# Optimization experiments

Hardware: AMD Instinct MI355X
Metric: run time of the kernel (lower is better)

Reference implementation:

```python
import jax, jax.numpy as jnp
import numpy as np

B, F, Q, CHUNK = 2, 8192, 4096, 512
NUM_VERTS = 6000


def _safe_div(n, d):
    return n / jnp.where(d == 0, 1.0, d)


def _bary(a, b, c, p):
    """Barycentric coords of the closest point on triangle (a,b,c) to p.
    All args broadcastable [..., 3]; returns [..., 3] (u, v, w) with
    closest = u*a + v*b + w*c. Ericson, Real-Time Collision Detection."""
    ab = b - a; ac = c - a; ap = p - a
    d1 = jnp.sum(ab * ap, -1); d2 = jnp.sum(ac * ap, -1)
    bp = p - b
    d3 = jnp.sum(ab * bp, -1); d4 = jnp.sum(ac * bp, -1)
    cp_ = p - c
    d5 = jnp.sum(ab * cp_, -1); d6 = jnp.sum(ac * cp_, -1)
    vc = d1 * d4 - d3 * d2
    vb = d5 * d2 - d1 * d6
    va = d3 * d6 - d5 * d4
    v_ab = _safe_div(d1, d1 - d3)
    w_ac = _safe_div(d2, d2 - d6)
    w_bc = _safe_div(d4 - d3, (d4 - d3) + (d5 - d6))
    inv = _safe_div(1.0, va + vb + vc)
    v_in = vb * inv; w_in = vc * inv
    zero = jnp.zeros_like(d1); one = jnp.ones_like(d1)
    conds = [(d1 <= 0) & (d2 <= 0),
             (d3 >= 0) & (d4 <= d3),
             (vc <= 0) & (d1 >= 0) & (d3 <= 0),
             (d6 >= 0) & (d5 <= d6),
             (vb <= 0) & (d2 >= 0) & (d6 <= 0),
             (va <= 0) & (d4 >= d3) & (d5 >= d6)]
    u = jnp.select(conds, [one, zero, 1 - v_ab, zero, 1 - w_ac, zero], 1 - v_in - w_in)
    v = jnp.select(conds, [zero, one, v_ab, zero, zero, 1 - w_bc], v_in)
    w = jnp.select(conds, [zero, zero, zero, one, w_ac, w_bc], w_in)
    return jnp.stack([u, v, w], -1)


def _closest_faces(triangles, points, chunk=CHUNK):
    """Exact closest-triangle index per query point (replaces BVH search).
    triangles [B,F,3,3], points [B,Q,3] -> int32 [B,Q]."""
    tri = jax.lax.stop_gradient(triangles)
    pts = jax.lax.stop_gradient(points)
    bsz, nq = pts.shape[0], pts.shape[1]
    a = tri[:, :, 0]; b = tri[:, :, 1]; c = tri[:, :, 2]  # [B,F,3]

    def one_chunk(p_chunk):  # [B,CH,3]
        pa = p_chunk[:, :, None, :]                       # [B,CH,1,3]
        bc = _bary(a[:, None], b[:, None], c[:, None], pa)  # [B,CH,F,3]
        cp = (bc[..., 0:1] * a[:, None] + bc[..., 1:2] * b[:, None]
              + bc[..., 2:3] * c[:, None])                # [B,CH,F,3]
        d2 = jnp.sum((cp - pa) ** 2, -1)                  # [B,CH,F]
        return jnp.argmin(d2, axis=-1)                    # [B,CH]

    chunks = jnp.moveaxis(pts.reshape(bsz, nq // chunk, chunk, 3), 1, 0)
    idx = jax.lax.map(one_chunk, chunks)                  # [NC,B,CH]
    return jnp.moveaxis(idx, 0, 1).reshape(bsz, nq)


def setup_inputs() -> dict:
    key = jax.random.key(0)
    k1, k2, k3, k4, k5 = jax.random.split(key, 5)
    return {
        'triangles': jax.random.normal(k1, (B, F, 3, 3), dtype=jnp.float32),
        'points': jax.random.normal(k2, (B, Q, 3), dtype=jnp.float32),
        'normals': jax.random.normal(k3, (B, F, 3, 3), dtype=jnp.float32),
        'cmaps': jax.random.normal(k4, (B, F, 3, 3), dtype=jnp.float32),
        'faces': jax.random.randint(k5, (B, F, 3), 0, NUM_VERTS, dtype=jnp.int32),
    }


def reference(triangles, points, normals, cmaps, faces):
    closest_faces = _closest_faces(triangles, points)     # [B,Q]
    idx = closest_faces[:, :, None, None]
    tri_g = jnp.take_along_axis(triangles, idx, axis=1)   # [B,Q,3,3]
    nrm_g = jnp.take_along_axis(normals, idx, axis=1)
    cmp_g = jnp.take_along_axis(cmaps, idx, axis=1)
    bcs = _bary(tri_g[:, :, 0], tri_g[:, :, 1], tri_g[:, :, 2], points)  # [B,Q,3]
    bcs = jnp.clip(bcs, 0.0, 1.0)
    closest_points = jnp.einsum('bqk,bqkd->bqd', bcs, tri_g)
    closest_normals = jnp.einsum('bqk,bqkd->bqd', bcs, nrm_g)
    closest_cmaps = jnp.einsum('bqk,bqkd->bqd', bcs, cmp_g)
    residual = closest_points - points
    closest_fids = jnp.take_along_axis(faces, closest_faces[:, :, None], axis=1)  # [B,Q,3]
    closest_idx = jnp.take_along_axis(
        closest_fids, jnp.argmax(bcs, -1)[:, :, None], axis=2)[..., 0]            # [B,Q]
    return residual, closest_normals, closest_cmaps, closest_idx
```

## Files before the change

kernel.cpp:

```cpp
#include <hip/hip_runtime.h>
#include <float.h>

#define B_   2
#define F_   8192
#define Q_   4096
#define NC   128
#define FC   (F_/NC)
#define PTS  256
#define PPT  2

typedef float f2 __attribute__((ext_vector_type(2)));
typedef unsigned int uint;

__device__ __forceinline__ f2 clamp01(f2 x) {
    f2 z = {0.f, 0.f}, o = {1.f, 1.f};
    return __builtin_elementwise_min(__builtin_elementwise_max(x, z), o);
}

__device__ __forceinline__ void bary_uvw(
    float ax, float ay, float az,
    float bx, float by, float bz,
    float cx, float cy, float cz,
    float px, float py, float pz,
    float& u, float& v, float& w)
{
#pragma clang fp contract(off)
    float abx = bx - ax, aby = by - ay, abz = bz - az;
    float acx = cx - ax, acy = cy - ay, acz = cz - az;
    float apx = px - ax, apy = py - ay, apz = pz - az;
    float d1 = abx*apx + aby*apy + abz*apz;
    float d2 = acx*apx + acy*apy + acz*apz;
    float bpx = px - bx, bpy = py - by, bpz = pz - bz;
    float d3 = abx*bpx + aby*bpy + abz*bpz;
    float d4 = acx*bpx + acy*bpy + acz*bpz;
    float qx = px - cx, qy = py - cy, qz = pz - cz;
    float d5 = abx*qx + aby*qy + abz*qz;
    float d6 = acx*qx + acy*qy + acz*qz;
    float vc = d1*d4 - d3*d2;
    float vb = d5*d2 - d1*d6;
    float va = d3*d6 - d5*d4;

    bool c1 = (d1 <= 0.f) && (d2 <= 0.f);
    bool c2 = (d3 >= 0.f) && (d4 <= d3);
    bool c3 = (vc <= 0.f) && (d1 >= 0.f) && (d3 <= 0.f);
    bool c4 = (d6 >= 0.f) && (d5 <= d6);
    bool c5 = (vb <= 0.f) && (d2 >= 0.f) && (d6 <= 0.f);
    bool c6 = (va <= 0.f) && (d4 >= d3) && (d5 >= d6);

    bool e1 = c1;
    bool p1 = !c1;
    bool e2 = p1 && c2;
    bool p2 = p1 && !c2;
    bool e3 = p2 && c3;
    bool p3 = p2 && !c3;
    bool e4 = p3 && c4;
    bool p4 = p3 && !c4;
    bool e5 = p4 && c5;
    bool p5 = p4 && !c5;
    bool e6 = p5 && c6;

    float d43 = d4 - d3;
    float d56 = d5 - d6;
    float n  = e3 ? d1        : (e5 ? d2        : (e6 ? d43         : 1.f));
    float dd = e3 ? (d1 - d3) : (e5 ? (d2 - d6) : (e6 ? (d43 + d56) : (va + vb + vc)));
    dd = (dd == 0.f) ? 1.f : dd;
    float t = n / dd;

    float vi = vb * t;
    float wi = vc * t;
    u = e1 ? 1.f : (e2 ? 0.f : (e3 ? 1.f - t : (e4 ? 0.f : (e5 ? 1.f - t : (e6 ? 0.f     : 1.f - vi - wi)))));
    v = e1 ? 0.f : (e2 ? 1.f : (e3 ? t       : (e4 ? 0.f : (e5 ? 0.f     : (e6 ? 1.f - t : vi)))));
    w = e1 ? 0.f : (e2 ? 0.f : (e3 ? 0.f     : (e4 ? 1.f : (e5 ? t       : (e6 ? t       : wi)))));
}

__global__ __launch_bounds__(PTS, 8) void scan_kernel(
    const float* __restrict__ tri, const float* __restrict__ pts,
    uint2* __restrict__ keys)
{
    __shared__ float4 S[FC * 4];
    const int tid = threadIdx.x;
    const int pb = blockIdx.x, cb = blockIdx.y, bb = blockIdx.z;

    {
        const int tr = tid & (FC - 1);
        const int qt = tid >> 6;
        const float* g = tri + ((size_t)bb * F_ + (size_t)cb * FC + tr) * 9;
        float ax = g[0], ay = g[1], az = g[2];
        float bx = g[3], by = g[4], bz = g[5];
        float cx = g[6], cy = g[7], cz = g[8];
        float abx = bx - ax, aby = by - ay, abz = bz - az;
        float acx = cx - ax, acy = cy - ay, acz = cz - az;
        float daa = abx*abx + aby*aby + abz*abz;
        float dcc = acx*acx + acy*acy + acz*acz;
        float dac = abx*acx + aby*acy + abz*acz;
        float4 v;
        if (qt == 0)      v = make_float4(ax, ay, az, daa);
        else if (qt == 1) v = make_float4(abx, aby, abz, dcc);
        else if (qt == 2) v = make_float4(acx, acy, acz, dac);
        else {
            float dbc = daa + dcc - 2.f*dac;
            float nn  = daa*dcc - dac*dac;
            v = make_float4(1.f/daa, 1.f/dcc, 1.f/dbc, 1.f/nn);
        }
        S[tr*4 + qt] = v;
    }
    __syncthreads();

    const int q0 = pb * (PTS * PPT) + tid * PPT;
    const float* p0 = pts + ((size_t)bb * Q_ + q0) * 3;
    f2 px = {p0[0], p0[3]};
    f2 py = {p0[1], p0[4]};
    f2 pz = {p0[2], p0[5]};

    uint a0 = 0xFFFFFFFFu, a1 = 0xFFFFFFFFu;
    uint b0 = 0xFFFFFFFFu, b1 = 0xFFFFFFFFu;
    #pragma unroll 2
    for (int fl = 0; fl < FC; ++fl) {
        float4 c0 = S[fl*4 + 0];
        float4 c1 = S[fl*4 + 1];
        float4 c2 = S[fl*4 + 2];
        float4 c3 = S[fl*4 + 3];
        float daa = c0.w, dcc = c1.w, dac = c2.w;
        float dbc = daa + dcc - 2.f*dac;
        float nn  = daa*dcc - dac*dac;
        float kk  = daa - dac;

        f2 apx = px - c0.x, apy = py - c0.y, apz = pz - c0.z;
        f2 d1  = c1.x*apx + c1.y*apy + c1.z*apz;
        f2 d2  = c2.x*apx + c2.y*apy + c2.z*apz;
        f2 app = apx*apx + apy*apy + apz*apz;
        f2 t1  = d1*dcc - d2*dac;
        f2 t2  = d2*daa - d1*dac;
        f2 t12 = t1 + t2;
        f2 sg  = d1*t1 + d2*t2;
        f2 dint = app - sg*c3.w;

        f2 d43 = (d2 - d1) + kk;
        f2 td1 = d1 + d1;
        f2 tab = clamp01(d1 * c3.x);
        f2 eab = app - tab*(td1 - tab*daa);
        f2 tac = clamp01(d2 * c3.y);
        f2 eac = app - tac*((d2 + d2) - tac*dcc);
        f2 bpp = (app - td1) + daa;
        f2 sbc = clamp01(d43 * c3.z);
        f2 ebc = bpp - sbc*((d43 + d43) - sbc*dbc);
        f2 emin = __builtin_elementwise_min(__builtin_elementwise_min(eab, eac), ebc);

        bool inA = (t1.x >= 0.f) & (t2.x >= 0.f) & (t12.x <= nn);
        bool inB = (t1.y >= 0.f) & (t2.y >= 0.f) & (t12.y <= nn);
        float dA = fmaxf(inA ? dint.x : emin.x, 0.f);
        float dB = fmaxf(inB ? dint.y : emin.y, 0.f);

        uint kA = (__float_as_uint(dA) & 0xFFFFFFC0u) | (uint)fl;
        uint kB = (__float_as_uint(dB) & 0xFFFFFFC0u) | (uint)fl;
        uint lo = min(a0, kA), hi = max(a0, kA);
        a0 = lo; a1 = min(a1, hi);
        lo = min(b0, kB); hi = max(b0, kB);
        b0 = lo; b1 = min(b1, hi);
    }

    size_t o = ((size_t)bb * Q_ + q0) * NC + cb;
    keys[o]      = make_uint2(a0, a1);
    keys[o + NC] = make_uint2(b0, b1);
}

__global__ __launch_bounds__(256) void finalize_kernel(
    const float* __restrict__ tri, const float* __restrict__ pts,
    const float* __restrict__ nrm, const float* __restrict__ cmp,
    const int* __restrict__ faces,
    const uint* __restrict__ keys,
    float* __restrict__ out)
{
#pragma clang fp contract(off)
    const int lane = threadIdx.x & 63;
    const int t = blockIdx.x * 4 + (threadIdx.x >> 6);
    const int bb = t / Q_;

    const float* pp = pts + (size_t)t * 3;
    float px = pp[0], py = pp[1], pz = pp[2];

    const uint4* kp = (const uint4*)keys;
    uint4 K = kp[(size_t)t * (NC/2) + lane];

    float dbest = FLT_MAX; int fbest = 0x7FFFFFFF;
    uint kj[4] = {K.x, K.y, K.z, K.w};
    #pragma unroll
    for (int j = 0; j < 4; ++j) {
        int face = (2*lane + (j >> 1)) * FC + (int)(kj[j] & 63u);
        const float* tg = tri + ((size_t)bb * F_ + face) * 9;
        float ax = tg[0], ay = tg[1], az = tg[2];
        float bx = tg[3], by = tg[4], bz = tg[5];
        float cx = tg[6], cy = tg[7], cz = tg[8];
        float u, v, w;
        bary_uvw(ax, ay, az, bx, by, bz, cx, cy, cz, px, py, pz, u, v, w);
        float cpx = u*ax + v*bx + w*cx;
        float cpy = u*ay + v*by + w*cy;
        float cpz = u*az + v*bz + w*cz;
        float dx = cpx - px, dy = cpy - py, dz = cpz - pz;
        float d2v = dx*dx + dy*dy + dz*dz;
        if (d2v < dbest || (d2v == dbest && face < fbest)) { dbest = d2v; fbest = face; }
    }
    for (int off = 32; off > 0; off >>= 1) {
        float od = __shfl_down(dbest, off);
        int   of = __shfl_down(fbest, off);
        if (od < dbest || (od == dbest && of < fbest)) { dbest = od; fbest = of; }
    }
    fbest = __shfl(fbest, 0);
    if (lane != 0) return;

    const int bestf = fbest;
    const float* tg = tri + ((size_t)bb * F_ + bestf) * 9;
    const float* ng = nrm + ((size_t)bb * F_ + bestf) * 9;
    const float* cg = cmp + ((size_t)bb * F_ + bestf) * 9;

    float u, v, w;
    bary_uvw(tg[0], tg[1], tg[2],  tg[3], tg[4], tg[5],  tg[6], tg[7], tg[8],
             px, py, pz, u, v, w);
    u = fminf(fmaxf(u, 0.f), 1.f);
    v = fminf(fmaxf(v, 0.f), 1.f);
    w = fminf(fmaxf(w, 0.f), 1.f);

    float cpx = u * tg[0] + v * tg[3] + w * tg[6];
    float cpy = u * tg[1] + v * tg[4] + w * tg[7];
    float cpz = u * tg[2] + v * tg[5] + w * tg[8];
    float nx  = u * ng[0] + v * ng[3] + w * ng[6];
    float ny  = u * ng[1] + v * ng[4] + w * ng[7];
    float nz  = u * ng[2] + v * ng[5] + w * ng[8];
    float mx  = u * cg[0] + v * cg[3] + w * cg[6];
    float my  = u * cg[1] + v * cg[4] + w * cg[7];
    float mz  = u * cg[2] + v * cg[5] + w * cg[8];

    const size_t S3 = (size_t)B_ * Q_ * 3;
    out[(size_t)t * 3 + 0] = cpx - px;
    out[(size_t)t * 3 + 1] = cpy - py;
    out[(size_t)t * 3 + 2] = cpz - pz;
    out[S3 + (size_t)t * 3 + 0] = nx;
    out[S3 + (size_t)t * 3 + 1] = ny;
    out[S3 + (size_t)t * 3 + 2] = nz;
    out[2 * S3 + (size_t)t * 3 + 0] = mx;
    out[2 * S3 + (size_t)t * 3 + 1] = my;
    out[2 * S3 + (size_t)t * 3 + 2] = mz;

    int k = 0; float mm = u;
    if (v > mm) { mm = v; k = 1; }
    if (w > mm) { k = 2; }
    out[3 * S3 + t] = (float)faces[((size_t)bb * F_ + bestf) * 3 + k];
}

extern "C" void kernel_launch(void* const* d_in, const int* in_sizes, int n_in,
                              void* d_out, int out_size, void* d_ws, size_t ws_size,
                              hipStream_t stream) {
    const float* tri   = (const float*)d_in[0];
    const float* pts   = (const float*)d_in[1];
    const float* nrm   = (const float*)d_in[2];
    const float* cmp   = (const float*)d_in[3];
    const int*   faces = (const int*)d_in[4];
    float* out = (float*)d_out;

    uint2* keys = (uint2*)d_ws;

    dim3 g1(Q_ / (PTS * PPT), NC, B_);
    scan_kernel<<<g1, PTS, 0, stream>>>(tri, pts, keys);
    finalize_kernel<<<(B_ * Q_) / 4, 256, 0, stream>>>(
        tri, pts, nrm, cmp, faces, (const uint*)keys, out);
}
```

Before: 155.2 us.

## Process four points per thread, restructure distance math, transpose key layout

The scan kernel now handles four query points per thread with half as many threads per block, so each shared-memory triangle record is reused across more points. The per-pair distance is rewritten as app minus a max-reduction, using reciprocal nn and a min-based inside test. The key buffer becomes chunk-major so the scan writes contiguous uint4 stores. The finalize kernel switches to vectorized unaligned loads for triangle, normal and cmap data. The trade-offs are higher register pressure and lower occupancy (launch bounds drop to 4), and small rounding differences in the distance test could change which faces end up as candidates.

```diff
diff --git a/kernel.cpp b/kernel.cpp
--- a/kernel.cpp
+++ b/kernel.cpp
@@ -6,10 +6,11 @@
 #define Q_   4096
 #define NC   128
 #define FC   (F_/NC)
-#define PTS  256
-#define PPT  2
+#define PTS  128
+#define PPT  4
 
 typedef float f2 __attribute__((ext_vector_type(2)));
+typedef float f4u __attribute__((ext_vector_type(4), aligned(4)));
 typedef unsigned int uint;
 
 __device__ __forceinline__ f2 clamp01(f2 x) {
@@ -73,7 +74,43 @@
     w = e1 ? 0.f : (e2 ? 0.f : (e3 ? 0.f     : (e4 ? 1.f : (e5 ? t       : (e6 ? t       : wi)))));
 }
 
-__global__ __launch_bounds__(PTS, 8) void scan_kernel(
+__device__ __forceinline__ f2 pair_dist(
+    f2 px, f2 py, f2 pz,
+    float ax, float ay, float az,
+    float abx, float aby, float abz,
+    float acx, float acy, float acz,
+    float daa, float dcc, float dac, float dbc, float kk,
+    float rdaa, float rdcc, float rdbc, float rnn)
+{
+    f2 apx = px - ax, apy = py - ay, apz = pz - az;
+    f2 d1  = abx*apx + aby*apy + abz*apz;
+    f2 d2  = acx*apx + acy*apy + acz*apz;
+    f2 app = apx*apx + apy*apy + apz*apz;
+
+    f2 t1 = d1*dcc - d2*dac;
+    f2 t2 = d2*daa - d1*dac;
+    f2 t12n = 1.f - (t1 + t2)*rnn;
+    f2 sgr  = (d1*t1 + d2*t2)*rnn;
+    f2 ins  = __builtin_elementwise_min(__builtin_elementwise_min(t1, t2), t12n);
+
+    f2 td1 = d1 + d1;
+    f2 tab = clamp01(d1 * rdaa);
+    f2 rab = tab*(td1 - tab*daa);
+    f2 tac = clamp01(d2 * rdcc);
+    f2 rac = tac*((d2 + d2) - tac*dcc);
+    f2 d43 = (d2 - d1) + kk;
+    f2 sbc = clamp01(d43 * rdbc);
+    f2 rbc = (td1 - daa) + sbc*((d43 + d43) - sbc*dbc);
+    f2 rmax = __builtin_elementwise_max(__builtin_elementwise_max(rab, rac), rbc);
+
+    f2 red;
+    red.x = (ins.x >= 0.f) ? sgr.x : rmax.x;
+    red.y = (ins.y >= 0.f) ? sgr.y : rmax.y;
+    f2 z = {0.f, 0.f};
+    return __builtin_elementwise_max(app - red, z);
+}
+
+__global__ __launch_bounds__(PTS, 4) void scan_kernel(
     const float* __restrict__ tri, const float* __restrict__ pts,
     uint2* __restrict__ keys)
 {
@@ -83,7 +120,7 @@
 
     {
         const int tr = tid & (FC - 1);
-        const int qt = tid >> 6;
+        const int hf = tid >> 6;
         const float* g = tri + ((size_t)bb * F_ + (size_t)cb * FC + tr) * 9;
         float ax = g[0], ay = g[1], az = g[2];
         float bx = g[3], by = g[4], bz = g[5];
@@ -93,27 +130,30 @@
         float daa = abx*abx + aby*aby + abz*abz;
         float dcc = acx*acx + acy*acy + acz*acz;
         float dac = abx*acx + aby*acy + abz*acz;
-        float4 v;
-        if (qt == 0)      v = make_float4(ax, ay, az, daa);
-        else if (qt == 1) v = make_float4(abx, aby, abz, dcc);
-        else if (qt == 2) v = make_float4(acx, acy, acz, dac);
-        else {
+        if (hf == 0) {
+            S[tr*4 + 0] = make_float4(ax, ay, az, daa);
+            S[tr*4 + 2] = make_float4(acx, acy, acz, dac);
+        } else {
             float dbc = daa + dcc - 2.f*dac;
             float nn  = daa*dcc - dac*dac;
-            v = make_float4(1.f/daa, 1.f/dcc, 1.f/dbc, 1.f/nn);
+            S[tr*4 + 1] = make_float4(abx, aby, abz, dcc);
+            S[tr*4 + 3] = make_float4(1.f/daa, 1.f/dcc, 1.f/dbc, 1.f/nn);
         }
-        S[tr*4 + qt] = v;
     }
     __syncthreads();
 
     const int q0 = pb * (PTS * PPT) + tid * PPT;
     const float* p0 = pts + ((size_t)bb * Q_ + q0) * 3;
-    f2 px = {p0[0], p0[3]};
-    f2 py = {p0[1], p0[4]};
-    f2 pz = {p0[2], p0[5]};
-
-    uint a0 = 0xFFFFFFFFu, a1 = 0xFFFFFFFFu;
-    uint b0 = 0xFFFFFFFFu, b1 = 0xFFFFFFFFu;
+    f4u l0 = *(const f4u*)(p0);
+    f4u l1 = *(const f4u*)(p0 + 4);
+    f4u l2 = *(const f4u*)(p0 + 8);
+    f2 pxA = {l0.x, l0.w}, pyA = {l0.y, l1.x}, pzA = {l0.z, l1.y};
+    f2 pxB = {l1.z, l2.y}, pyB = {l1.w, l2.z}, pzB = {l2.x, l2.w};
+
+    uint k00 = 0xFFFFFFFFu, k01 = 0xFFFFFFFFu;
+    uint k10 = 0xFFFFFFFFu, k11 = 0xFFFFFFFFu;
+    uint k20 = 0xFFFFFFFFu, k21 = 0xFFFFFFFFu;
+    uint k30 = 0xFFFFFFFFu, k31 = 0xFFFFFFFFu;
     #pragma unroll 2
     for (int fl = 0; fl < FC; ++fl) {
         float4 c0 = S[fl*4 + 0];
@@ -122,75 +162,72 @@
         float4 c3 = S[fl*4 + 3];
         float daa = c0.w, dcc = c1.w, dac = c2.w;
         float dbc = daa + dcc - 2.f*dac;
-        float nn  = daa*dcc - dac*dac;
         float kk  = daa - dac;
 
-        f2 apx = px - c0.x, apy = py - c0.y, apz = pz - c0.z;
-        f2 d1  = c1.x*apx + c1.y*apy + c1.z*apz;
-        f2 d2  = c2.x*apx + c2.y*apy + c2.z*apz;
-        f2 app = apx*apx + apy*apy + apz*apz;
-        f2 t1  = d1*dcc - d2*dac;
-        f2 t2  = d2*daa - d1*dac;
-        f2 t12 = t1 + t2;
-        f2 sg  = d1*t1 + d2*t2;
-        f2 dint = app - sg*c3.w;
-
-        f2 d43 = (d2 - d1) + kk;
-        f2 td1 = d1 + d1;
-        f2 tab = clamp01(d1 * c3.x);
-        f2 eab = app - tab*(td1 - tab*daa);
-        f2 tac = clamp01(d2 * c3.y);
-        f2 eac = app - tac*((d2 + d2) - tac*dcc);
-        f2 bpp = (app - td1) + daa;
-        f2 sbc = clamp01(d43 * c3.z);
-        f2 ebc = bpp - sbc*((d43 + d43) - sbc*dbc);
-        f2 emin = __builtin_elementwise_min(__builtin_elementwise_min(eab, eac), ebc);
-
-        bool inA = (t1.x >= 0.f) & (t2.x >= 0.f) & (t12.x <= nn);
-        bool inB = (t1.y >= 0.f) & (t2.y >= 0.f) & (t12.y <= nn);
-        float dA = fmaxf(inA ? dint.x : emin.x, 0.f);
-        float dB = fmaxf(inB ? dint.y : emin.y, 0.f);
-
-        uint kA = (__float_as_uint(dA) & 0xFFFFFFC0u) | (uint)fl;
-        uint kB = (__float_as_uint(dB) & 0xFFFFFFC0u) | (uint)fl;
-        uint lo = min(a0, kA), hi = max(a0, kA);
-        a0 = lo; a1 = min(a1, hi);
-        lo = min(b0, kB); hi = max(b0, kB);
-        b0 = lo; b1 = min(b1, hi);
-    }
-
-    size_t o = ((size_t)bb * Q_ + q0) * NC + cb;
-    keys[o]      = make_uint2(a0, a1);
-    keys[o + NC] = make_uint2(b0, b1);
+        f2 dA = pair_dist(pxA, pyA, pzA, c0.x, c0.y, c0.z,
+                          c1.x, c1.y, c1.z, c2.x, c2.y, c2.z,
+                          daa, dcc, dac, dbc, kk, c3.x, c3.y, c3.z, c3.w);
+        f2 dB = pair_dist(pxB, pyB, pzB, c0.x, c0.y, c0.z,
+                          c1.x, c1.y, c1.z, c2.x, c2.y, c2.z,
+                          daa, dcc, dac, dbc, kk, c3.x, c3.y, c3.z, c3.w);
+
+        uint kA0 = (__float_as_uint(dA.x) & 0xFFFFFFC0u) | (uint)fl;
+        uint kA1 = (__float_as_uint(dA.y) & 0xFFFFFFC0u) | (uint)fl;
+        uint kB0 = (__float_as_uint(dB.x) & 0xFFFFFFC0u) | (uint)fl;
+        uint kB1 = (__float_as_uint(dB.y) & 0xFFFFFFC0u) | (uint)fl;
+        uint lo, hi;
+        lo = min(k00, kA0); hi = max(k00, kA0); k00 = lo; k01 = min(k01, hi);
+        lo = min(k10, kA1); hi = max(k10, kA1); k10 = lo; k11 = min(k11, hi);
+        lo = min(k20, kB0); hi = max(k20, kB0); k20 = lo; k21 = min(k21, hi);
+        lo = min(k30, kB1); hi = max(k30, kB1); k30 = lo; k31 = min(k31, hi);
+    }
+
+    size_t idx = ((size_t)(bb * NC + cb) * Q_ + q0);
+    uint4* k4 = (uint4*)&keys[idx];
+    k4[0] = make_uint4(k00, k01, k10, k11);
+    k4[1] = make_uint4(k20, k21, k30, k31);
 }
 
 __global__ __launch_bounds__(256) void finalize_kernel(
     const float* __restrict__ tri, const float* __restrict__ pts,
     const float* __restrict__ nrm, const float* __restrict__ cmp,
     const int* __restrict__ faces,
-    const uint* __restrict__ keys,
+    const uint2* __restrict__ keys,
     float* __restrict__ out)
 {
 #pragma clang fp contract(off)
     const int lane = threadIdx.x & 63;
     const int t = blockIdx.x * 4 + (threadIdx.x >> 6);
-    const int bb = t / Q_;
+    const int bb = t >> 12;
+    const int q  = t & (Q_ - 1);
 
     const float* pp = pts + (size_t)t * 3;
     float px = pp[0], py = pp[1], pz = pp[2];
 
-    const uint4* kp = (const uint4*)keys;
-    uint4 K = kp[(size_t)t * (NC/2) + lane];
-
-    float dbest = FLT_MAX; int fbest = 0x7FFFFFFF;
-    uint kj[4] = {K.x, K.y, K.z, K.w};
+    uint2 kc0 = keys[((size_t)(bb * NC + 2*lane    ) * Q_ + q)];
+    uint2 kc1 = keys[((size_t)(bb * NC + 2*lane + 1) * Q_ + q)];
+
+    int face[4];
+    face[0] = (2*lane    ) * FC + (int)(kc0.x & 63u);
+    face[1] = (2*lane    ) * FC + (int)(kc0.y & 63u);
+    face[2] = (2*lane + 1) * FC + (int)(kc1.x & 63u);
+    face[3] = (2*lane + 1) * FC + (int)(kc1.y & 63u);
+
+    f4u A[4], Bv[4]; float Cs[4];
     #pragma unroll
     for (int j = 0; j < 4; ++j) {
-        int face = (2*lane + (j >> 1)) * FC + (int)(kj[j] & 63u);
-        const float* tg = tri + ((size_t)bb * F_ + face) * 9;
-        float ax = tg[0], ay = tg[1], az = tg[2];
-        float bx = tg[3], by = tg[4], bz = tg[5];
-        float cx = tg[6], cy = tg[7], cz = tg[8];
+        const float* tg = tri + ((size_t)bb * F_ + face[j]) * 9;
+        A[j]  = *(const f4u*)(tg);
+        Bv[j] = *(const f4u*)(tg + 4);
+        Cs[j] = tg[8];
+    }
+
+    float dbest = FLT_MAX; int fbest = 0x7FFFFFFF;
+    #pragma unroll
+    for (int j = 0; j < 4; ++j) {
+        float ax = A[j].x, ay = A[j].y, az = A[j].z;
+        float bx = A[j].w, by = Bv[j].x, bz = Bv[j].y;
+        float cx = Bv[j].z, cy = Bv[j].w, cz = Cs[j];
         float u, v, w;
         bary_uvw(ax, ay, az, bx, by, bz, cx, cy, cz, px, py, pz, u, v, w);
         float cpx = u*ax + v*bx + w*cx;
@@ -198,7 +235,8 @@
         float cpz = u*az + v*bz + w*cz;
         float dx = cpx - px, dy = cpy - py, dz = cpz - pz;
         float d2v = dx*dx + dy*dy + dz*dz;
-        if (d2v < dbest || (d2v == dbest && face < fbest)) { dbest = d2v; fbest = face; }
+        int fj = face[j];
+        if (d2v < dbest || (d2v == dbest && fj < fbest)) { dbest = d2v; fbest = fj; }
     }
     for (int off = 32; off > 0; off >>= 1) {
         float od = __shfl_down(dbest, off);
@@ -212,23 +250,29 @@
     const float* tg = tri + ((size_t)bb * F_ + bestf) * 9;
     const float* ng = nrm + ((size_t)bb * F_ + bestf) * 9;
     const float* cg = cmp + ((size_t)bb * F_ + bestf) * 9;
+    f4u TA = *(const f4u*)(tg), TB = *(const f4u*)(tg + 4);
+    float TC = tg[8];
+    f4u NA = *(const f4u*)(ng), NB = *(const f4u*)(ng + 4);
+    float NCs = ng[8];
+    f4u CA = *(const f4u*)(cg), CB = *(const f4u*)(cg + 4);
+    float CC = cg[8];
 
     float u, v, w;
-    bary_uvw(tg[0], tg[1], tg[2],  tg[3], tg[4], tg[5],  tg[6], tg[7], tg[8],
+    bary_uvw(TA.x, TA.y, TA.z, TA.w, TB.x, TB.y, TB.z, TB.w, TC,
              px, py, pz, u, v, w);
     u = fminf(fmaxf(u, 0.f), 1.f);
     v = fminf(fmaxf(v, 0.f), 1.f);
     w = fminf(fmaxf(w, 0.f), 1.f);
 
-    float cpx = u * tg[0] + v * tg[3] + w * tg[6];
-    float cpy = u * tg[1] + v * tg[4] + w * tg[7];
-    float cpz = u * tg[2] + v * tg[5] + w * tg[8];
-    float nx  = u * ng[0] + v * ng[3] + w * ng[6];
-    float ny  = u * ng[1] + v * ng[4] + w * ng[7];
-    float nz  = u * ng[2] + v * ng[5] + w * ng[8];
-    float mx  = u * cg[0] + v * cg[3] + w * cg[6];
-    float my  = u * cg[1] + v * cg[4] + w * cg[7];
-    float mz  = u * cg[2] + v * cg[5] + w * cg[8];
+    float cpx = u * TA.x + v * TA.w + w * TB.z;
+    float cpy = u * TA.y + v * TB.x + w * TB.w;
+    float cpz = u * TA.z + v * TB.y + w * TC;
+    float nx  = u * NA.x + v * NA.w + w * NB.z;
+    float ny  = u * NA.y + v * NB.x + w * NB.w;
+    float nz  = u * NA.z + v * NB.y + w * NCs;
+    float mx  = u * CA.x + v * CA.w + w * CB.z;
+    float my  = u * CA.y + v * CB.x + w * CB.w;
+    float mz  = u * CA.z + v * CB.y + w * CC;
 
     const size_t S3 = (size_t)B_ * Q_ * 3;
     out[(size_t)t * 3 + 0] = cpx - px;
@@ -262,5 +306,5 @@
     dim3 g1(Q_ / (PTS * PPT), NC, B_);
     scan_kernel<<<g1, PTS, 0, stream>>>(tri, pts, keys);
     finalize_kernel<<<(B_ * Q_) / 4, 256, 0, stream>>>(
-        tri, pts, nrm, cmp, faces, (const uint*)keys, out);
-}
+        tri, pts, nrm, cmp, faces, keys, out);
+}
```

Result: faster. 148.1 us (-4.5%).
